# Optimization experiments

Measured on AMD Instinct MI355X. Metric: run time of the kernel, lower is better.

Reference implementation:

```python
import jax, jax.numpy as jnp
import numpy as np

N_HEAD = 4

def setup_inputs() -> dict:
    key = jax.random.key(0)
    ks = jax.random.split(key, 5)
    B, T, C = 2, 4096, 64
    return {
        "x": jax.random.normal(ks[0], (B, T, C), dtype=jnp.float32),
        "w_attn": jax.random.normal(ks[1], (3 * C, C), dtype=jnp.float32) * 0.02,
        "b_attn": jax.random.normal(ks[2], (3 * C,), dtype=jnp.float32) * 0.02,
        "w_proj": jax.random.normal(ks[3], (C, C), dtype=jnp.float32) * 0.02,
        "b_proj": jax.random.normal(ks[4], (C,), dtype=jnp.float32) * 0.02,
    }

def reference(x, w_attn, b_attn, w_proj, b_proj):
    B, T, C = x.shape
    H = N_HEAD
    Dh = C // H
    # fused QKV projection (torch Linear: x @ W.T + b)
    qkv = x @ w_attn.T + b_attn                      # [B,T,3C]
    q, k, v = jnp.split(qkv, 3, axis=-1)             # each [B,T,C]
    q = q.reshape(B, T, H, Dh).transpose(0, 2, 1, 3)  # [B,H,T,Dh]
    k = k.reshape(B, T, H, Dh).transpose(0, 2, 1, 3)
    v = v.reshape(B, T, H, Dh).transpose(0, 2, 1, 3)
    scale = 1.0 / np.sqrt(Dh).astype(np.float32)
    scores = jnp.einsum("bhqd,bhkd->bhqk", q, k) * scale  # [B,H,T,T]
    attn = jax.nn.softmax(scores, axis=-1)
    y = jnp.einsum("bhqk,bhkd->bhqd", attn, v)       # [B,H,T,Dh]
    y = y.transpose(0, 2, 1, 3).reshape(B, T, C)     # [B,T,C]
    return y @ w_proj.T + b_proj
```

## Files before the change

kernel.cpp:

```cpp
#include <hip/hip_runtime.h>
#include <math.h>

#define BB 2
#define TT 4096
#define CC 64
#define HH 4
#define DH 16
#define NROW (BB*TT)
#define SCALE 0.36067376022224085f

typedef __fp16 h4 __attribute__((ext_vector_type(4)));
typedef __fp16 h2 __attribute__((ext_vector_type(2)));
typedef float  f4 __attribute__((ext_vector_type(4)));

__global__ __launch_bounds__(256) void qkv_kernel(const float* __restrict__ x,
        const float* __restrict__ w, const float* __restrict__ bias,
        __fp16* __restrict__ Q, __fp16* __restrict__ K, __fp16* __restrict__ VT) {
    __shared__ __fp16 smv[64][16];
    const int t = threadIdx.x;
    const int wave = t >> 6, lane = t & 63;
    const int lq = lane & 15, g = lane >> 4;
    const int r0 = blockIdx.x*16;
    const int b = r0 >> 12, tt0 = r0 & (TT-1);

    h4 xb[4];
    const float* xrow = x + (size_t)(r0 + lq)*CC;
    #pragma unroll
    for (int s = 0; s < 4; s++) {
        float4 xv = *(const float4*)(xrow + s*16 + g*4);
        h2 lo = __builtin_amdgcn_cvt_pkrtz(xv.x, xv.y);
        h2 hi = __builtin_amdgcn_cvt_pkrtz(xv.z, xv.w);
        xb[s] = (h4){lo.x, lo.y, hi.x, hi.y};
    }

    #pragma unroll
    for (int j = 0; j < 3; j++) {
        const int nt = wave*3 + j;
        const int o0 = nt*16;
        const float sc = (nt < 4) ? SCALE : 1.0f;
        float4 bv = *(const float4*)(bias + o0 + g*4);
        f4 acc = {bv.x*sc, bv.y*sc, bv.z*sc, bv.w*sc};
        #pragma unroll
        for (int s = 0; s < 4; s++) {
            float4 wv = *(const float4*)(w + (size_t)(o0 + lq)*CC + s*16 + g*4);
            h2 lo = __builtin_amdgcn_cvt_pkrtz(wv.x*sc, wv.y*sc);
            h2 hi = __builtin_amdgcn_cvt_pkrtz(wv.z*sc, wv.w*sc);
            h4 af = (h4){lo.x, lo.y, hi.x, hi.y};
            acc = __builtin_amdgcn_mfma_f32_16x16x16f16(af, xb[s], acc, 0, 0, 0);
        }
        h2 plo = __builtin_amdgcn_cvt_pkrtz(acc.x, acc.y);
        h2 phi = __builtin_amdgcn_cvt_pkrtz(acc.z, acc.w);
        h4 pk = (h4){plo.x, plo.y, phi.x, phi.y};
        if (nt < 8) {
            const int part = nt >> 2, h = nt & 3;
            __fp16* dst = (part == 0) ? Q : K;
            *(h4*)(dst + ((size_t)(b*HH + h)*TT + tt0 + lq)*DH + g*4) = pk;
        } else {
            const int h = nt - 8;
            smv[h*16 + g*4 + 0][lq] = pk.x;
            smv[h*16 + g*4 + 1][lq] = pk.y;
            smv[h*16 + g*4 + 2][lq] = pk.z;
            smv[h*16 + g*4 + 3][lq] = pk.w;
        }
    }
    __syncthreads();
    if (t < 64) {
        const int h = t >> 4, d = t & 15;
        uint4 v0 = *(const uint4*)&smv[t][0];
        uint4 v1 = *(const uint4*)&smv[t][8];
        __fp16* dst = VT + (size_t)(b*HH + h)*TT*DH
                        + (size_t)((tt0 >> 6)*16 + d)*64 + (tt0 & 63);
        *(uint4*)dst = v0;
        *(uint4*)(dst + 8) = v1;
    }
}

__global__ __launch_bounds__(512) void attn_kernel(const __fp16* __restrict__ Q,
        const __fp16* __restrict__ K, const __fp16* __restrict__ VT,
        __fp16* __restrict__ yh) {
    __shared__ f4    Osm[4][4][64];
    __shared__ float Lsm[4][4][64];
    const int t = threadIdx.x;
    const int wave = t >> 6, lane = t & 63;
    const int lq = lane & 15, g = lane >> 4;
    const int head = blockIdx.x >> 6;
    const int qt   = blockIdx.x & 63;
    const int q0 = qt*64;
    const __fp16* Qh = Q  + (size_t)head*TT*DH;
    const __fp16* Kh = K  + (size_t)head*TT*DH;
    const __fp16* Vh = VT + (size_t)head*TT*DH;

    h4 qf[4];
    #pragma unroll
    for (int h = 0; h < 4; h++)
        qf[h] = *(const h4*)(Qh + (size_t)(q0 + h*16 + lq)*DH + g*4);

    f4 O[4];
    float lp[4];
    #pragma unroll
    for (int h = 0; h < 4; h++) { O[h] = (f4){0.f,0.f,0.f,0.f}; lp[h] = 0.f; }

    const __fp16* kp = Kh + (size_t)(wave*512 + lq)*DH + g*4;
    const __fp16* vp = Vh + (size_t)(wave*8)*1024 + lq*64 + g*4;

    h4 ka[4], va[4], kb[4], vb[4];
    #pragma unroll
    for (int s = 0; s < 4; s++) {
        ka[s] = *(const h4*)(kp + (size_t)s*16*DH);
        va[s] = *(const h4*)(vp + s*16);
    }

#define ATTN_CHUNK(KF, VF)                                                        \
    {                                                                             \
        const f4 z = {0.f, 0.f, 0.f, 0.f};                                        \
        _Pragma("unroll")                                                         \
        for (int h = 0; h < 4; h++) {                                             \
            f4 S0 = __builtin_amdgcn_mfma_f32_16x16x16f16(KF[0], qf[h], z, 0,0,0);\
            f4 S1 = __builtin_amdgcn_mfma_f32_16x16x16f16(KF[1], qf[h], z, 0,0,0);\
            f4 S2 = __builtin_amdgcn_mfma_f32_16x16x16f16(KF[2], qf[h], z, 0,0,0);\
            f4 S3 = __builtin_amdgcn_mfma_f32_16x16x16f16(KF[3], qf[h], z, 0,0,0);\
            float p0, p1, p2, p3; h2 lo, hi; h4 P; float lacc = 0.f;              \
            p0 = __builtin_amdgcn_exp2f(S0.x); p1 = __builtin_amdgcn_exp2f(S0.y); \
            p2 = __builtin_amdgcn_exp2f(S0.z); p3 = __builtin_amdgcn_exp2f(S0.w); \
            lacc += p0 + p1 + p2 + p3;                                            \
            lo = __builtin_amdgcn_cvt_pkrtz(p0, p1);                              \
            hi = __builtin_amdgcn_cvt_pkrtz(p2, p3);                              \
            P = (h4){lo.x, lo.y, hi.x, hi.y};                                     \
            O[h] = __builtin_amdgcn_mfma_f32_16x16x16f16(VF[0], P, O[h], 0,0,0);  \
            p0 = __builtin_amdgcn_exp2f(S1.x); p1 = __builtin_amdgcn_exp2f(S1.y); \
            p2 = __builtin_amdgcn_exp2f(S1.z); p3 = __builtin_amdgcn_exp2f(S1.w); \
            lacc += p0 + p1 + p2 + p3;                                            \
            lo = __builtin_amdgcn_cvt_pkrtz(p0, p1);                              \
            hi = __builtin_amdgcn_cvt_pkrtz(p2, p3);                              \
            P = (h4){lo.x, lo.y, hi.x, hi.y};                                     \
            O[h] = __builtin_amdgcn_mfma_f32_16x16x16f16(VF[1], P, O[h], 0,0,0);  \
            p0 = __builtin_amdgcn_exp2f(S2.x); p1 = __builtin_amdgcn_exp2f(S2.y); \
            p2 = __builtin_amdgcn_exp2f(S2.z); p3 = __builtin_amdgcn_exp2f(S2.w); \
            lacc += p0 + p1 + p2 + p3;                                            \
            lo = __builtin_amdgcn_cvt_pkrtz(p0, p1);                              \
            hi = __builtin_amdgcn_cvt_pkrtz(p2, p3);                              \
            P = (h4){lo.x, lo.y, hi.x, hi.y};                                     \
            O[h] = __builtin_amdgcn_mfma_f32_16x16x16f16(VF[2], P, O[h], 0,0,0);  \
            p0 = __builtin_amdgcn_exp2f(S3.x); p1 = __builtin_amdgcn_exp2f(S3.y); \
            p2 = __builtin_amdgcn_exp2f(S3.z); p3 = __builtin_amdgcn_exp2f(S3.w); \
            lacc += p0 + p1 + p2 + p3;                                            \
            lo = __builtin_amdgcn_cvt_pkrtz(p0, p1);                              \
            hi = __builtin_amdgcn_cvt_pkrtz(p2, p3);                              \
            P = (h4){lo.x, lo.y, hi.x, hi.y};                                     \
            O[h] = __builtin_amdgcn_mfma_f32_16x16x16f16(VF[3], P, O[h], 0,0,0);  \
            lp[h] += lacc;                                                        \
        }                                                                         \
    }

    for (int step = 0; step < 8; step += 2) {
        {
            const __fp16* kp1 = kp + (size_t)(step + 1)*64*DH;
            const __fp16* vp1 = vp + (size_t)(step + 1)*1024;
            #pragma unroll
            for (int s = 0; s < 4; s++) {
                kb[s] = *(const h4*)(kp1 + (size_t)s*16*DH);
                vb[s] = *(const h4*)(vp1 + s*16);
            }
        }
        ATTN_CHUNK(ka, va)
        {
            const int c2 = (step + 2 < 8) ? step + 2 : 7;
            const __fp16* kp2 = kp + (size_t)c2*64*DH;
            const __fp16* vp2 = vp + (size_t)c2*1024;
            #pragma unroll
            for (int s = 0; s < 4; s++) {
                ka[s] = *(const h4*)(kp2 + (size_t)s*16*DH);
                va[s] = *(const h4*)(vp2 + s*16);
            }
        }
        ATTN_CHUNK(kb, vb)
    }
#undef ATTN_CHUNK

    if (wave >= 4) {
        #pragma unroll
        for (int h = 0; h < 4; h++) {
            Osm[wave-4][h][lane] = O[h];
            Lsm[wave-4][h][lane] = lp[h];
        }
    }
    __syncthreads();
    if (wave < 4) {
        #pragma unroll
        for (int h = 0; h < 4; h++) {
            O[h] += Osm[wave][h][lane];
            lp[h] += Lsm[wave][h][lane];
        }
    }
    __syncthreads();
    if (wave < 4) {
        #pragma unroll
        for (int h = 0; h < 4; h++) {
            Osm[wave][h][lane] = O[h];
            Lsm[wave][h][lane] = lp[h];
        }
    }
    __syncthreads();
    if (wave < 4) {
        f4 Os = Osm[0][wave][lane];
        Os += Osm[1][wave][lane];
        Os += Osm[2][wave][lane];
        Os += Osm[3][wave][lane];
        float L = 0.f;
        #pragma unroll
        for (int ks = 0; ks < 4; ks++)
            #pragma unroll
            for (int gg = 0; gg < 4; gg++)
                L += Lsm[ks][wave][gg*16 + lq];
        const float rinv = 1.f / L;
        h2 lo = __builtin_amdgcn_cvt_pkrtz(Os.x*rinv, Os.y*rinv);
        h2 hi = __builtin_amdgcn_cvt_pkrtz(Os.z*rinv, Os.w*rinv);
        h4 pk = (h4){lo.x, lo.y, hi.x, hi.y};
        const int b = head >> 2, hh = head & 3;
        *(h4*)(yh + ((size_t)b*TT + q0 + wave*16 + lq)*CC + hh*DH + g*4) = pk;
    }
}

__global__ __launch_bounds__(256) void proj_kernel(const __fp16* __restrict__ yh,
        const float* __restrict__ w, const float* __restrict__ bias,
        float* __restrict__ out) {
    const int t = threadIdx.x;
    const int wave = t >> 6, lane = t & 63;
    const int lq = lane & 15, g = lane >> 4;
    const int r0 = blockIdx.x*16;
    const int o0 = wave*16;

    h4 yb[4];
    const __fp16* yrow = yh + (size_t)(r0 + lq)*CC;
    #pragma unroll
    for (int s = 0; s < 4; s++) yb[s] = *(const h4*)(yrow + s*16 + g*4);

    float4 bv = *(const float4*)(bias + o0 + g*4);
    f4 acc = {bv.x, bv.y, bv.z, bv.w};
    #pragma unroll
    for (int s = 0; s < 4; s++) {
        float4 wv = *(const float4*)(w + (size_t)(o0 + lq)*CC + s*16 + g*4);
        h2 lo = __builtin_amdgcn_cvt_pkrtz(wv.x, wv.y);
        h2 hi = __builtin_amdgcn_cvt_pkrtz(wv.z, wv.w);
        h4 af = (h4){lo.x, lo.y, hi.x, hi.y};
        acc = __builtin_amdgcn_mfma_f32_16x16x16f16(af, yb[s], acc, 0, 0, 0);
    }
    *(float4*)(out + (size_t)(r0 + lq)*CC + o0 + g*4) = (float4){acc.x, acc.y, acc.z, acc.w};
}

extern "C" void kernel_launch(void* const* d_in, const int* in_sizes, int n_in,
                              void* d_out, int out_size, void* d_ws, size_t ws_size,
                              hipStream_t stream) {
    const float* x      = (const float*)d_in[0];
    const float* w_attn = (const float*)d_in[1];
    const float* b_attn = (const float*)d_in[2];
    const float* w_proj = (const float*)d_in[3];
    const float* b_proj = (const float*)d_in[4];
    float* out = (float*)d_out;

    const size_t headsz = (size_t)BB*HH*TT*DH;
    __fp16* Q   = (__fp16*)d_ws;
    __fp16* K   = Q + headsz;
    __fp16* VT  = K + headsz;
    __fp16* yh  = VT + headsz;

    qkv_kernel<<<NROW/16, 256, 0, stream>>>(x, w_attn, b_attn, Q, K, VT);
    attn_kernel<<<BB*HH*(TT/64), 512, 0, stream>>>(Q, K, VT, yh);
    proj_kernel<<<NROW/16, 256, 0, stream>>>(yh, w_proj, b_proj, out);
}
```

Measured before the change: 95.94 us.

## Use 4-wave attention blocks with longer key ranges and staggered chunk order

The attention kernel now runs 256 threads (4 waves) per block instead of 8. Each wave covers 1024 keys in 16 chunks rather than 512 keys in 8, which removes the two-stage cross-wave reduction and two barriers. Chunk traversal starts at a rotated offset per block and wave, meant to spread concurrent K/V reads across memory. The trade-off is fewer waves per block for hiding latency and a longer serial loop per wave.

```diff
diff --git a/kernel.cpp b/kernel.cpp
--- a/kernel.cpp
+++ b/kernel.cpp
@@ -75,7 +75,7 @@
     }
 }
 
-__global__ __launch_bounds__(512) void attn_kernel(const __fp16* __restrict__ Q,
+__global__ __launch_bounds__(256) void attn_kernel(const __fp16* __restrict__ Q,
         const __fp16* __restrict__ K, const __fp16* __restrict__ VT,
         __fp16* __restrict__ yh) {
     __shared__ f4    Osm[4][4][64];
@@ -100,14 +100,19 @@
     #pragma unroll
     for (int h = 0; h < 4; h++) { O[h] = (f4){0.f,0.f,0.f,0.f}; lp[h] = 0.f; }
 
-    const __fp16* kp = Kh + (size_t)(wave*512 + lq)*DH + g*4;
-    const __fp16* vp = Vh + (size_t)(wave*8)*1024 + lq*64 + g*4;
+    const __fp16* kbase = Kh + (size_t)(wave*1024 + lq)*DH + g*4;
+    const __fp16* vbase = Vh + (size_t)(wave*16)*1024 + lq*64 + g*4;
+
+    const int start = (blockIdx.x*5 + wave*3) & 15;
 
     h4 ka[4], va[4], kb[4], vb[4];
-    #pragma unroll
-    for (int s = 0; s < 4; s++) {
-        ka[s] = *(const h4*)(kp + (size_t)s*16*DH);
-        va[s] = *(const h4*)(vp + s*16);
+    {
+        const int c0 = start;
+        #pragma unroll
+        for (int s = 0; s < 4; s++) {
+            ka[s] = *(const h4*)(kbase + (size_t)c0*64*DH + (size_t)s*16*DH);
+            va[s] = *(const h4*)(vbase + (size_t)c0*1024 + s*16);
+        }
     }
 
 #define ATTN_CHUNK(KF, VF)                                                        \
@@ -152,73 +157,51 @@
         }                                                                         \
     }
 
-    for (int step = 0; step < 8; step += 2) {
+    for (int it = 0; it < 16; it += 2) {
         {
-            const __fp16* kp1 = kp + (size_t)(step + 1)*64*DH;
-            const __fp16* vp1 = vp + (size_t)(step + 1)*1024;
+            const int c1 = (start + it + 1) & 15;
             #pragma unroll
             for (int s = 0; s < 4; s++) {
-                kb[s] = *(const h4*)(kp1 + (size_t)s*16*DH);
-                vb[s] = *(const h4*)(vp1 + s*16);
+                kb[s] = *(const h4*)(kbase + (size_t)c1*64*DH + (size_t)s*16*DH);
+                vb[s] = *(const h4*)(vbase + (size_t)c1*1024 + s*16);
             }
         }
         ATTN_CHUNK(ka, va)
         {
-            const int c2 = (step + 2 < 8) ? step + 2 : 7;
-            const __fp16* kp2 = kp + (size_t)c2*64*DH;
-            const __fp16* vp2 = vp + (size_t)c2*1024;
+            const int c2 = (start + it + 2) & 15;
             #pragma unroll
             for (int s = 0; s < 4; s++) {
-                ka[s] = *(const h4*)(kp2 + (size_t)s*16*DH);
-                va[s] = *(const h4*)(vp2 + s*16);
+                ka[s] = *(const h4*)(kbase + (size_t)c2*64*DH + (size_t)s*16*DH);
+                va[s] = *(const h4*)(vbase + (size_t)c2*1024 + s*16);
             }
         }
         ATTN_CHUNK(kb, vb)
     }
 #undef ATTN_CHUNK
 
-    if (wave >= 4) {
+    #pragma unroll
+    for (int h = 0; h < 4; h++) {
+        Osm[wave][h][lane] = O[h];
+        Lsm[wave][h][lane] = lp[h];
+    }
+    __syncthreads();
+
+    f4 Os = Osm[0][wave][lane];
+    Os += Osm[1][wave][lane];
+    Os += Osm[2][wave][lane];
+    Os += Osm[3][wave][lane];
+    float L = 0.f;
+    #pragma unroll
+    for (int ks = 0; ks < 4; ks++)
         #pragma unroll
-        for (int h = 0; h < 4; h++) {
-            Osm[wave-4][h][lane] = O[h];
-            Lsm[wave-4][h][lane] = lp[h];
-        }
-    }
-    __syncthreads();
-    if (wave < 4) {
-        #pragma unroll
-        for (int h = 0; h < 4; h++) {
-            O[h] += Osm[wave][h][lane];
-            lp[h] += Lsm[wave][h][lane];
-        }
-    }
-    __syncthreads();
-    if (wave < 4) {
-        #pragma unroll
-        for (int h = 0; h < 4; h++) {
-            Osm[wave][h][lane] = O[h];
-            Lsm[wave][h][lane] = lp[h];
-        }
-    }
-    __syncthreads();
-    if (wave < 4) {
-        f4 Os = Osm[0][wave][lane];
-        Os += Osm[1][wave][lane];
-        Os += Osm[2][wave][lane];
-        Os += Osm[3][wave][lane];
-        float L = 0.f;
-        #pragma unroll
-        for (int ks = 0; ks < 4; ks++)
-            #pragma unroll
-            for (int gg = 0; gg < 4; gg++)
-                L += Lsm[ks][wave][gg*16 + lq];
-        const float rinv = 1.f / L;
-        h2 lo = __builtin_amdgcn_cvt_pkrtz(Os.x*rinv, Os.y*rinv);
-        h2 hi = __builtin_amdgcn_cvt_pkrtz(Os.z*rinv, Os.w*rinv);
-        h4 pk = (h4){lo.x, lo.y, hi.x, hi.y};
-        const int b = head >> 2, hh = head & 3;
-        *(h4*)(yh + ((size_t)b*TT + q0 + wave*16 + lq)*CC + hh*DH + g*4) = pk;
-    }
+        for (int gg = 0; gg < 4; gg++)
+            L += Lsm[ks][wave][gg*16 + lq];
+    const float rinv = 1.f / L;
+    h2 lo = __builtin_amdgcn_cvt_pkrtz(Os.x*rinv, Os.y*rinv);
+    h2 hi = __builtin_amdgcn_cvt_pkrtz(Os.z*rinv, Os.w*rinv);
+    h4 pk = (h4){lo.x, lo.y, hi.x, hi.y};
+    const int b = head >> 2, hh = head & 3;
+    *(h4*)(yh + ((size_t)b*TT + q0 + wave*16 + lq)*CC + hh*DH + g*4) = pk;
 }
 
 __global__ __launch_bounds__(256) void proj_kernel(const __fp16* __restrict__ yh,
@@ -265,6 +248,6 @@
     __fp16* yh  = VT + headsz;
 
     qkv_kernel<<<NROW/16, 256, 0, stream>>>(x, w_attn, b_attn, Q, K, VT);
-    attn_kernel<<<BB*HH*(TT/64), 512, 0, stream>>>(Q, K, VT, yh);
+    attn_kernel<<<BB*HH*(TT/64), 256, 0, stream>>>(Q, K, VT, yh);
     proj_kernel<<<NROW/16, 256, 0, stream>>>(yh, w_proj, b_proj, out);
 }
```

Measured after the change: 95.05 us. No clear change (-0.9%).
